# Kernel tuning notes

Hardware: AMD Instinct MI355X
Metric: run time of the kernel (lower is better)

## Reference

```python
import jax, jax.numpy as jnp
import numpy as np

NUM_NODE_TYPES = 8
HIDDEN = 64
D = 4
N_NODES = 100000
N_EDGES = 3200000
LN_EPS = 1e-5


def setup_inputs() -> dict:
    key = jax.random.key(0)
    ks = jax.random.split(key, 8)
    total_in = 2 * NUM_NODE_TYPES
    out_dim = D * D
    x = jax.random.normal(ks[0], (N_NODES, 16), dtype=jnp.float32)
    edge_index = jax.random.randint(ks[1], (2, N_EDGES), 0, N_NODES, dtype=jnp.int64)
    node_types = jax.random.randint(ks[2], (N_NODES,), 0, NUM_NODE_TYPES, dtype=jnp.int64)
    # LayerNorm params
    ln_g = jnp.ones((total_in,), dtype=jnp.float32)
    ln_b = jnp.zeros((total_in,), dtype=jnp.float32)
    # Linear layers (kaiming-ish init)
    W1 = jax.random.normal(ks[3], (total_in, HIDDEN), dtype=jnp.float32) * (1.0 / np.sqrt(total_in))
    b1 = jnp.zeros((HIDDEN,), dtype=jnp.float32)
    W2 = jax.random.normal(ks[4], (HIDDEN, out_dim), dtype=jnp.float32) * (1.0 / np.sqrt(HIDDEN))
    b2 = jnp.zeros((out_dim,), dtype=jnp.float32)
    return {"x": x, "edge_index": edge_index, "node_types": node_types,
            "ln_g": ln_g, "ln_b": ln_b, "W1": W1, "b1": b1, "W2": W2, "b2": b2}


def reference(x, edge_index, node_types, ln_g, ln_b, W1, b1, W2, b2):
    row, col = edge_index[0], edge_index[1]
    # one-hot node types then per-edge gather of src/tgt types
    onehot = jax.nn.one_hot(node_types, NUM_NODE_TYPES, dtype=jnp.float32)  # [N, T]
    h = jnp.concatenate([onehot[row], onehot[col]], axis=-1)  # [E, 2T]
    # LayerNorm
    mu = jnp.mean(h, axis=-1, keepdims=True)
    var = jnp.mean(jnp.square(h - mu), axis=-1, keepdims=True)
    hn = (h - mu) * jax.lax.rsqrt(var + LN_EPS) * ln_g + ln_b
    # MLP
    h1 = jax.nn.relu(hn @ W1 + b1)          # [E, HIDDEN]
    h_sheaf = (h1 @ W2 + b2).reshape(-1, D, D)  # [E, d, d]
    attention_maps = jax.nn.softmax(h_sheaf, axis=-1)
    sheaf_maps = jnp.eye(D, dtype=h_sheaf.dtype)[None] - attention_maps
    return sheaf_maps
```

## Files before the change

kernel.cpp:

```cpp
#include <hip/hip_runtime.h>
#include <math.h>

#define NUM_T   8
#define TIN     16
#define HID     64
#define OUTD    16
#define LN_EPS  1e-5f

#define N_PACK_U32  12500
#define PACK_BLOCKS 49

typedef float f32x4 __attribute__((ext_vector_type(4)));

__global__ __launch_bounds__(256) void
prep_kernel(const int* __restrict__ ntypes, int n_nodes,
            const float* __restrict__ ln_g,
            const float* __restrict__ ln_b,
            const float* __restrict__ W1,
            const float* __restrict__ b1,
            const float* __restrict__ W2,
            const float* __restrict__ b2,
            f32x4* __restrict__ table4,
            unsigned int* __restrict__ packed)
{
    const int t = threadIdx.x;

    if (blockIdx.x < PACK_BLOCKS) {
        const int g = blockIdx.x * 256 + t;
        if (g < N_PACK_U32) {
            unsigned int w = 0;
            int n0 = g * 8;
            #pragma unroll
            for (int j = 0; j < 8; ++j) {
                int n = n0 + j;
                unsigned int ty = (n < n_nodes) ? (unsigned int)ntypes[n] : 0u;
                w |= (ty & 7u) << (j * 4);
            }
            packed[g] = w;
        }
        return;
    }

    if (t >= 64) return;
    const int p  = blockIdx.x - PACK_BLOCKS;
    const int ts = p >> 3;
    const int tt = p & 7;
    const int k  = t;

    const float mu = 2.0f / 16.0f;
    float var = 0.0f;
    #pragma unroll
    for (int j = 0; j < TIN; ++j) {
        float h = (j == ts || j == (8 + tt)) ? 1.0f : 0.0f;
        float d = h - mu;
        var += d * d;
    }
    var *= (1.0f / 16.0f);
    const float inv = rsqrtf(var + LN_EPS);

    float a = b1[k];
    #pragma unroll
    for (int j = 0; j < TIN; ++j) {
        float h  = (j == ts || j == (8 + tt)) ? 1.0f : 0.0f;
        float hn = (h - mu) * inv * ln_g[j] + ln_b[j];
        a += hn * W1[j * HID + k];
    }
    a = fmaxf(a, 0.0f);

    const f32x4* W2v = (const f32x4*)W2;
    f32x4 w0 = W2v[k * 4 + 0], w1 = W2v[k * 4 + 1],
          w2 = W2v[k * 4 + 2], w3 = W2v[k * 4 + 3];

    float s[OUTD];
    #pragma unroll
    for (int i = 0; i < 4; ++i) {
        s[0 + i]  = a * w0[i];
        s[4 + i]  = a * w1[i];
        s[8 + i]  = a * w2[i];
        s[12 + i] = a * w3[i];
    }
    #pragma unroll
    for (int o = 0; o < OUTD; ++o) {
        s[o] += __shfl_xor(s[o], 1);
        s[o] += __shfl_xor(s[o], 2);
        s[o] += __shfl_xor(s[o], 4);
        s[o] += __shfl_xor(s[o], 8);
        s[o] += __shfl_xor(s[o], 16);
        s[o] += __shfl_xor(s[o], 32);
        s[o] += b2[o];
    }

    if (t < 4) {
        const int r = t;
        float s0 = s[4*r+0], s1 = s[4*r+1], s2 = s[4*r+2], s3 = s[4*r+3];
        float m  = fmaxf(fmaxf(s0, s1), fmaxf(s2, s3));
        float e0 = expf(s0 - m), e1 = expf(s1 - m),
              e2 = expf(s2 - m), e3 = expf(s3 - m);
        float rs = 1.0f / (e0 + e1 + e2 + e3);
        f32x4 outv;
        outv.x = (r == 0 ? 1.0f : 0.0f) - e0 * rs;
        outv.y = (r == 1 ? 1.0f : 0.0f) - e1 * rs;
        outv.z = (r == 2 ? 1.0f : 0.0f) - e2 * rs;
        outv.w = (r == 3 ? 1.0f : 0.0f) - e3 * rs;
        table4[p * 4 + r] = outv;
    }
}

template <bool EXACT>
__global__ __launch_bounds__(1024) void
scatter_edges_kernel(const int* __restrict__ row,
                     const int* __restrict__ col,
                     const unsigned int* __restrict__ packed,
                     const f32x4* __restrict__ table4,
                     f32x4* __restrict__ out4,
                     int E)
{
    __shared__ f32x4 lds_table[64 * 5];
    __shared__ unsigned int nt_lds[N_PACK_U32];

    const int t = threadIdx.x;

    if (t < 256) {
        int p = t >> 2, q = t & 3;
        lds_table[p * 5 + q] = table4[t];
    }
    {
        const uint4* s4 = (const uint4*)packed;
        uint4* d4 = (uint4*)nt_lds;
        for (int i = t; i < N_PACK_U32 / 4; i += 1024) d4[i] = s4[i];
    }
    __syncthreads();

    const int lane = t & 63;
    const int wid  = t >> 6;
    const int q    = lane & 3;
    const int sub  = lane >> 2;
    const int stride = gridDim.x * 1024;

    int base = blockIdx.x * 1024 + wid * 64;
    if (base >= E) return;

    int pair;
    {
        int e  = base + lane;
        int ec = EXACT ? e : ((e < E) ? e : (E - 1));
        int r = row[ec];
        int c = col[ec];
        unsigned int tr = (nt_lds[r >> 3] >> ((r & 7) * 4)) & 7u;
        unsigned int tc = (nt_lds[c >> 3] >> ((c & 7) * 4)) & 7u;
        pair = (int)((tr << 3) | tc);
    }

    while (base < E) {
        const int nbase = base + stride;
        const bool have_next = (nbase < E);

        int rn = 0, cn = 0;
        if (have_next) {
            int en  = nbase + lane;
            int enc = EXACT ? en : ((en < E) ? en : (E - 1));
            rn = row[enc];
            cn = col[enc];
        }

        #pragma unroll
        for (int j = 0; j < 4; ++j) {
            int src = j * 16 + sub;
            int pj  = __shfl(pair, src, 64);
            if (EXACT) {
                out4[(base + src) * 4 + q] = lds_table[pj * 5 + q];
            } else {
                int ej = base + src;
                if (ej < E) out4[ej * 4 + q] = lds_table[pj * 5 + q];
            }
        }

        if (have_next) {
            unsigned int tr = (nt_lds[rn >> 3] >> ((rn & 7) * 4)) & 7u;
            unsigned int tc = (nt_lds[cn >> 3] >> ((cn & 7) * 4)) & 7u;
            pair = (int)((tr << 3) | tc);
        }
        base = nbase;
    }
}

extern "C" void kernel_launch(void* const* d_in, const int* in_sizes, int n_in,
                              void* d_out, int out_size, void* d_ws, size_t ws_size,
                              hipStream_t stream)
{
    const int*   edge_index = (const int*)d_in[1];
    const int*   ntypes     = (const int*)d_in[2];
    const float* ln_g       = (const float*)d_in[3];
    const float* ln_b       = (const float*)d_in[4];
    const float* W1         = (const float*)d_in[5];
    const float* b1         = (const float*)d_in[6];
    const float* W2         = (const float*)d_in[7];
    const float* b2         = (const float*)d_in[8];

    const int E = in_sizes[1] / 2;
    const int N = in_sizes[2];

    f32x4*        table4 = (f32x4*)d_ws;
    unsigned int* packed = (unsigned int*)((char*)d_ws + 4096);

    prep_kernel<<<PACK_BLOCKS + 64, 256, 0, stream>>>(
        ntypes, N, ln_g, ln_b, W1, b1, W2, b2, table4, packed);

    const int blocks = 512;
    if ((E & 63) == 0) {
        scatter_edges_kernel<true><<<blocks, 1024, 0, stream>>>(
            edge_index, edge_index + E, packed, table4, (f32x4*)d_out, E);
    } else {
        scatter_edges_kernel<false><<<blocks, 1024, 0, stream>>>(
            edge_index, edge_index + E, packed, table4, (f32x4*)d_out, E);
    }
}
```

Baseline: 45.99 us.

## Build lookup table inside scatter blocks and use nontemporal output stores

The 64-entry sheaf-map table is no longer computed by the prep kernel. Each scatter block now builds it redundantly in LDS, with 16 waves each handling 4 type pairs. This removes the table work and the workspace round-trip from the first launch, which now only packs node types. Output stores become nontemporal so the large streamed output is less likely to pollute the cache. The cost is redundant MLP work in all 512 blocks before the main loop starts, and more registers and shuffles in the scatter kernel.

```diff
diff --git a/kernel.cpp b/kernel.cpp
--- a/kernel.cpp
+++ b/kernel.cpp
@@ -13,96 +13,95 @@
 typedef float f32x4 __attribute__((ext_vector_type(4)));
 
 __global__ __launch_bounds__(256) void
-prep_kernel(const int* __restrict__ ntypes, int n_nodes,
-            const float* __restrict__ ln_g,
-            const float* __restrict__ ln_b,
-            const float* __restrict__ W1,
-            const float* __restrict__ b1,
-            const float* __restrict__ W2,
-            const float* __restrict__ b2,
-            f32x4* __restrict__ table4,
+pack_kernel(const int* __restrict__ ntypes, int n_nodes,
             unsigned int* __restrict__ packed)
 {
-    const int t = threadIdx.x;
-
-    if (blockIdx.x < PACK_BLOCKS) {
-        const int g = blockIdx.x * 256 + t;
-        if (g < N_PACK_U32) {
-            unsigned int w = 0;
-            int n0 = g * 8;
+    const int g = blockIdx.x * 256 + threadIdx.x;
+    if (g < N_PACK_U32) {
+        unsigned int w = 0;
+        int n0 = g * 8;
+        #pragma unroll
+        for (int j = 0; j < 8; ++j) {
+            int n = n0 + j;
+            unsigned int ty = (n < n_nodes) ? (unsigned int)ntypes[n] : 0u;
+            w |= (ty & 7u) << (j * 4);
+        }
+        packed[g] = w;
+    }
+}
+
+__device__ __forceinline__ void
+build_table_inblock(int wid, int lane,
+                    const float* __restrict__ ln_g,
+                    const float* __restrict__ ln_b,
+                    const float* __restrict__ W1,
+                    const float* __restrict__ b1,
+                    const float* __restrict__ W2,
+                    const float* __restrict__ b2,
+                    f32x4* lds_table )
+{
+    const int k = lane;
+    const f32x4* W2v = (const f32x4*)W2;
+
+    #pragma unroll
+    for (int pi = 0; pi < 4; ++pi) {
+        const int p  = wid * 4 + pi;
+        const int ts = p >> 3;
+        const int tt = p & 7;
+
+        const float mu = 2.0f / 16.0f;
+        float var = 0.0f;
+        #pragma unroll
+        for (int j = 0; j < TIN; ++j) {
+            float h = (j == ts || j == (8 + tt)) ? 1.0f : 0.0f;
+            float d = h - mu;
+            var += d * d;
+        }
+        var *= (1.0f / 16.0f);
+        const float inv = rsqrtf(var + LN_EPS);
+
+        float a = b1[k];
+        #pragma unroll
+        for (int j = 0; j < TIN; ++j) {
+            float h  = (j == ts || j == (8 + tt)) ? 1.0f : 0.0f;
+            float hn = (h - mu) * inv * ln_g[j] + ln_b[j];
+            a += hn * W1[j * HID + k];
+        }
+        a = fmaxf(a, 0.0f);
+
+        #pragma unroll
+        for (int h = 0; h < 2; ++h) {
+            f32x4 wlo = W2v[k * 4 + 2 * h];
+            f32x4 whi = W2v[k * 4 + 2 * h + 1];
+            float s[8];
             #pragma unroll
-            for (int j = 0; j < 8; ++j) {
-                int n = n0 + j;
-                unsigned int ty = (n < n_nodes) ? (unsigned int)ntypes[n] : 0u;
-                w |= (ty & 7u) << (j * 4);
+            for (int i = 0; i < 4; ++i) { s[i] = a * wlo[i]; s[4 + i] = a * whi[i]; }
+            #pragma unroll
+            for (int o = 0; o < 8; ++o) {
+                s[o] += __shfl_xor(s[o], 1);
+                s[o] += __shfl_xor(s[o], 2);
+                s[o] += __shfl_xor(s[o], 4);
+                s[o] += __shfl_xor(s[o], 8);
+                s[o] += __shfl_xor(s[o], 16);
+                s[o] += __shfl_xor(s[o], 32);
+                s[o] += b2[8 * h + o];
             }
-            packed[g] = w;
-        }
-        return;
-    }
-
-    if (t >= 64) return;
-    const int p  = blockIdx.x - PACK_BLOCKS;
-    const int ts = p >> 3;
-    const int tt = p & 7;
-    const int k  = t;
-
-    const float mu = 2.0f / 16.0f;
-    float var = 0.0f;
-    #pragma unroll
-    for (int j = 0; j < TIN; ++j) {
-        float h = (j == ts || j == (8 + tt)) ? 1.0f : 0.0f;
-        float d = h - mu;
-        var += d * d;
-    }
-    var *= (1.0f / 16.0f);
-    const float inv = rsqrtf(var + LN_EPS);
-
-    float a = b1[k];
-    #pragma unroll
-    for (int j = 0; j < TIN; ++j) {
-        float h  = (j == ts || j == (8 + tt)) ? 1.0f : 0.0f;
-        float hn = (h - mu) * inv * ln_g[j] + ln_b[j];
-        a += hn * W1[j * HID + k];
-    }
-    a = fmaxf(a, 0.0f);
-
-    const f32x4* W2v = (const f32x4*)W2;
-    f32x4 w0 = W2v[k * 4 + 0], w1 = W2v[k * 4 + 1],
-          w2 = W2v[k * 4 + 2], w3 = W2v[k * 4 + 3];
-
-    float s[OUTD];
-    #pragma unroll
-    for (int i = 0; i < 4; ++i) {
-        s[0 + i]  = a * w0[i];
-        s[4 + i]  = a * w1[i];
-        s[8 + i]  = a * w2[i];
-        s[12 + i] = a * w3[i];
-    }
-    #pragma unroll
-    for (int o = 0; o < OUTD; ++o) {
-        s[o] += __shfl_xor(s[o], 1);
-        s[o] += __shfl_xor(s[o], 2);
-        s[o] += __shfl_xor(s[o], 4);
-        s[o] += __shfl_xor(s[o], 8);
-        s[o] += __shfl_xor(s[o], 16);
-        s[o] += __shfl_xor(s[o], 32);
-        s[o] += b2[o];
-    }
-
-    if (t < 4) {
-        const int r = t;
-        float s0 = s[4*r+0], s1 = s[4*r+1], s2 = s[4*r+2], s3 = s[4*r+3];
-        float m  = fmaxf(fmaxf(s0, s1), fmaxf(s2, s3));
-        float e0 = expf(s0 - m), e1 = expf(s1 - m),
-              e2 = expf(s2 - m), e3 = expf(s3 - m);
-        float rs = 1.0f / (e0 + e1 + e2 + e3);
-        f32x4 outv;
-        outv.x = (r == 0 ? 1.0f : 0.0f) - e0 * rs;
-        outv.y = (r == 1 ? 1.0f : 0.0f) - e1 * rs;
-        outv.z = (r == 2 ? 1.0f : 0.0f) - e2 * rs;
-        outv.w = (r == 3 ? 1.0f : 0.0f) - e3 * rs;
-        table4[p * 4 + r] = outv;
+            if (lane < 2) {
+                const int r  = 2 * h + lane;
+                const int o0 = 4 * lane;
+                float s0 = s[o0+0], s1 = s[o0+1], s2 = s[o0+2], s3 = s[o0+3];
+                float m  = fmaxf(fmaxf(s0, s1), fmaxf(s2, s3));
+                float e0 = expf(s0 - m), e1 = expf(s1 - m),
+                      e2 = expf(s2 - m), e3 = expf(s3 - m);
+                float rs = 1.0f / (e0 + e1 + e2 + e3);
+                f32x4 outv;
+                outv.x = (r == 0 ? 1.0f : 0.0f) - e0 * rs;
+                outv.y = (r == 1 ? 1.0f : 0.0f) - e1 * rs;
+                outv.z = (r == 2 ? 1.0f : 0.0f) - e2 * rs;
+                outv.w = (r == 3 ? 1.0f : 0.0f) - e3 * rs;
+                lds_table[p * 5 + r] = outv;
+            }
+        }
     }
 }
 
@@ -111,28 +110,30 @@
 scatter_edges_kernel(const int* __restrict__ row,
                      const int* __restrict__ col,
                      const unsigned int* __restrict__ packed,
-                     const f32x4* __restrict__ table4,
+                     const float* __restrict__ ln_g,
+                     const float* __restrict__ ln_b,
+                     const float* __restrict__ W1,
+                     const float* __restrict__ b1,
+                     const float* __restrict__ W2,
+                     const float* __restrict__ b2,
                      f32x4* __restrict__ out4,
                      int E)
 {
     __shared__ f32x4 lds_table[64 * 5];
     __shared__ unsigned int nt_lds[N_PACK_U32];
 
-    const int t = threadIdx.x;
-
-    if (t < 256) {
-        int p = t >> 2, q = t & 3;
-        lds_table[p * 5 + q] = table4[t];
-    }
+    const int t    = threadIdx.x;
+    const int lane = t & 63;
+    const int wid  = t >> 6;
+
     {
         const uint4* s4 = (const uint4*)packed;
         uint4* d4 = (uint4*)nt_lds;
         for (int i = t; i < N_PACK_U32 / 4; i += 1024) d4[i] = s4[i];
     }
+    build_table_inblock(wid, lane, ln_g, ln_b, W1, b1, W2, b2, lds_table);
     __syncthreads();
 
-    const int lane = t & 63;
-    const int wid  = t >> 6;
     const int q    = lane & 3;
     const int sub  = lane >> 2;
     const int stride = gridDim.x * 1024;
@@ -168,10 +169,14 @@
             int src = j * 16 + sub;
             int pj  = __shfl(pair, src, 64);
             if (EXACT) {
-                out4[(base + src) * 4 + q] = lds_table[pj * 5 + q];
+                f32x4 v = lds_table[pj * 5 + q];
+                __builtin_nontemporal_store(v, &out4[(base + src) * 4 + q]);
             } else {
                 int ej = base + src;
-                if (ej < E) out4[ej * 4 + q] = lds_table[pj * 5 + q];
+                if (ej < E) {
+                    f32x4 v = lds_table[pj * 5 + q];
+                    __builtin_nontemporal_store(v, &out4[ej * 4 + q]);
+                }
             }
         }
 
@@ -200,18 +205,18 @@
     const int E = in_sizes[1] / 2;
     const int N = in_sizes[2];
 
-    f32x4*        table4 = (f32x4*)d_ws;
-    unsigned int* packed = (unsigned int*)((char*)d_ws + 4096);
-
-    prep_kernel<<<PACK_BLOCKS + 64, 256, 0, stream>>>(
-        ntypes, N, ln_g, ln_b, W1, b1, W2, b2, table4, packed);
+    unsigned int* packed = (unsigned int*)d_ws;
+
+    pack_kernel<<<PACK_BLOCKS, 256, 0, stream>>>(ntypes, N, packed);
 
     const int blocks = 512;
     if ((E & 63) == 0) {
         scatter_edges_kernel<true><<<blocks, 1024, 0, stream>>>(
-            edge_index, edge_index + E, packed, table4, (f32x4*)d_out, E);
+            edge_index, edge_index + E, packed,
+            ln_g, ln_b, W1, b1, W2, b2, (f32x4*)d_out, E);
     } else {
         scatter_edges_kernel<false><<<blocks, 1024, 0, stream>>>(
-            edge_index, edge_index + E, packed, table4, (f32x4*)d_out, E);
-    }
-}
+            edge_index, edge_index + E, packed,
+            ln_g, ln_b, W1, b1, W2, b2, (f32x4*)d_out, E);
+    }
+}
```

Result: slower. 82.32 us (+79.0%).
